# Kernel tuning notes

Measured on AMD Instinct MI355X. Metric: run time of the kernel, lower is better.

Reference implementation:

```python
import jax, jax.numpy as jnp
import numpy as np
from jax import lax

EMBED_DIM = 128
N_RELATIONS = 64
N_ENTITIES = 100000
N_EDGES = 600000


def setup_inputs() -> dict:
    key = jax.random.key(0)
    k1, k2, k3, k4, k5, k6 = jax.random.split(key, 6)
    entity_emb = jax.random.normal(k1, (N_ENTITIES, EMBED_DIM), dtype=jnp.float32)
    heads = jax.random.randint(k2, (N_EDGES,), 0, N_ENTITIES)
    rels = jax.random.randint(k3, (N_EDGES,), 0, N_RELATIONS)
    tails = jax.random.randint(k4, (N_EDGES,), 0, N_ENTITIES)
    # learned params: relation embedding table (std=0.01) and square Linear weight (xavier)
    rel_embed_weight = 0.01 * jax.random.normal(k5, (N_RELATIONS, EMBED_DIM), dtype=jnp.float32)
    xavier = float(np.sqrt(6.0 / (EMBED_DIM + EMBED_DIM)))
    W = jax.random.uniform(k6, (EMBED_DIM, EMBED_DIM), dtype=jnp.float32, minval=-xavier, maxval=xavier)
    return {"entity_emb": entity_emb, "rel_embed_weight": rel_embed_weight, "W": W,
            "heads": heads, "rels": rels, "tails": tails}


def reference(entity_emb, rel_embed_weight, W, heads, rels, tails):
    n_entities = entity_emb.shape[0]
    # gather edge endpoint / relation embeddings: [E, D]
    e_h = entity_emb[heads]
    e_t = entity_emb[tails]
    e_r = rel_embed_weight[rels]
    # tanh-gated dot-product score per edge: [E]
    score = jnp.sum(e_t * jnp.tanh(e_h + e_r), axis=-1)
    # global max-shift (detached in torch) then per-head segment softmax
    score_exp = jnp.exp(score - lax.stop_gradient(jnp.max(score)))
    score_sum = jax.ops.segment_sum(score_exp, heads, num_segments=n_entities)
    attn = score_exp / (score_sum[heads] + 1e-10)
    # scatter-add attention-weighted messages back to head nodes: [N, D]
    agg = jax.ops.segment_sum(attn[:, None] * e_t, heads, num_segments=n_entities)
    # final Linear (no bias) + LeakyReLU(0.2); dropout is identity in eval mode
    out = (entity_emb + agg) @ W.T
    return jax.nn.leaky_relu(out, negative_slope=0.2)
```

## Files before the change

kernel.cpp:

```cpp
#include <hip/hip_runtime.h>
#include <math.h>

#define EMBED 128
#define BMAX 8192
#define LDSPAD 136
#define DBINS 64

#define TWO_LOG2E 2.8853900817779268f
#define DEFER_THR 32.0f

typedef __attribute__((ext_vector_type(8))) short short8;
typedef __attribute__((ext_vector_type(4))) float floatx4;

__device__ __forceinline__ float ex2(float x) { return __builtin_amdgcn_exp2f(x); }

__device__ __forceinline__ float fast_tanh2(float x) {
    float e = ex2(TWO_LOG2E * x);
    return 1.0f - 2.0f * __builtin_amdgcn_rcpf(1.0f + e);
}

__device__ __forceinline__ unsigned short f2b(float f) {
    union { float f; unsigned int u; } v; v.f = f;
    unsigned int r = v.u + 0x7FFFu + ((v.u >> 16) & 1u);
    return (unsigned short)(r >> 16);
}

__device__ __forceinline__ float b2f(short u) {
    union { float f; unsigned int i; } v;
    v.i = ((unsigned int)(unsigned short)u) << 16;
    return v.f;
}

template <int CTRL>
__device__ __forceinline__ float dpp_add_f(float x) {
    int y = __builtin_amdgcn_update_dpp(0, __float_as_int(x), CTRL, 0xF, 0xF, false);
    return x + __int_as_float(y);
}
__device__ __forceinline__ float dpp_sum16(float s) {
    s = dpp_add_f<0x121>(s);
    s = dpp_add_f<0x122>(s);
    s = dpp_add_f<0x124>(s);
    s = dpp_add_f<0x128>(s);
    return s;
}

__global__ __launch_bounds__(256) void k_cast_hist(
    const float* __restrict__ ent, const float* __restrict__ rel, const float* __restrict__ W,
    short* __restrict__ entb, short* __restrict__ relb, short* __restrict__ wb,
    const int* __restrict__ heads, int* __restrict__ cnt, int* __restrict__ ghist,
    int ngE, int ngR, int ngW, int E)
{
    if (blockIdx.x == 0 && threadIdx.x < DBINS) ghist[threadIdx.x] = 0;
    int stride = gridDim.x * 256;
    int total = ngE + ngR + ngW;
    for (int g = blockIdx.x * 256 + threadIdx.x; g < total; g += stride) {
        const float4* src; short* dst;
        if (g < ngE)            { src = (const float4*)ent + (size_t)g * 2;              dst = entb + (size_t)g * 8; }
        else if (g < ngE + ngR) { int g2 = g - ngE;       src = (const float4*)rel + (size_t)g2 * 2; dst = relb + (size_t)g2 * 8; }
        else                    { int g2 = g - ngE - ngR; src = (const float4*)W   + (size_t)g2 * 2; dst = wb   + (size_t)g2 * 8; }
        float4 a = src[0], b = src[1];
        short8 o;
        o[0] = (short)f2b(a.x); o[1] = (short)f2b(a.y); o[2] = (short)f2b(a.z); o[3] = (short)f2b(a.w);
        o[4] = (short)f2b(b.x); o[5] = (short)f2b(b.y); o[6] = (short)f2b(b.z); o[7] = (short)f2b(b.w);
        *(short8*)dst = o;
    }
    for (int e = blockIdx.x * 256 + threadIdx.x; e < E; e += stride)
        atomicAdd(cnt + heads[e], 1);
}

__global__ __launch_bounds__(1024) void k_scan1(
    const int* __restrict__ cnt, int* __restrict__ offs,
    int* __restrict__ bsum, int* __restrict__ ghist, int N)
{
    __shared__ int wsum[16];
    __shared__ int dh[DBINS];
    const int tid = threadIdx.x;
    if (tid < DBINS) dh[tid] = 0;
    int i = blockIdx.x * 1024 + tid;
    int v = (i < N) ? cnt[i] : 0;
    __syncthreads();
    if (i < N) atomicAdd(&dh[v < DBINS ? v : DBINS - 1], 1);
    int x = v;
    #pragma unroll
    for (int d = 1; d < 64; d <<= 1) {
        int y = __shfl_up(x, d, 64);
        if ((tid & 63) >= d) x += y;
    }
    if ((tid & 63) == 63) wsum[tid >> 6] = x;
    __syncthreads();
    if (tid < 16) {
        int w = wsum[tid];
        #pragma unroll
        for (int d = 1; d < 16; d <<= 1) {
            int y = __shfl_up(w, d, 16);
            if (tid >= d) w += y;
        }
        wsum[tid] = w;
    }
    __syncthreads();
    int add = (tid >= 64) ? wsum[(tid >> 6) - 1] : 0;
    int incl = x + add;
    if (i < N) offs[i] = incl - v;
    if (tid == 1023) bsum[blockIdx.x] = incl;
    if (tid < DBINS && dh[tid] > 0) atomicAdd(ghist + tid, dh[tid]);
}

__global__ __launch_bounds__(256) void k_scan23(
    int* __restrict__ offs, const int* __restrict__ bsum,
    int* __restrict__ cursor, const int* __restrict__ cnt,
    const int* __restrict__ ghist, int* __restrict__ bincur,
    int* __restrict__ order, int N, int nb)
{
    __shared__ int sb[256];
    __shared__ int ws4[4];
    __shared__ int dbs[DBINS];
    __shared__ int lcnt[DBINS];
    __shared__ int lbase[DBINS];
    const int tid = threadIdx.x;

    int v = (tid < nb) ? bsum[tid] : 0;
    int x = v;
    #pragma unroll
    for (int d = 1; d < 64; d <<= 1) {
        int y = __shfl_up(x, d, 64);
        if ((tid & 63) >= d) x += y;
    }
    if ((tid & 63) == 63) ws4[tid >> 6] = x;
    __syncthreads();
    if (tid < 4) {
        int w = ws4[tid];
        #pragma unroll
        for (int d = 1; d < 4; d <<= 1) {
            int y = __shfl_up(w, d, 4);
            if (tid >= d) w += y;
        }
        ws4[tid] = w;
    }
    __syncthreads();
    int add = (tid >= 64) ? ws4[(tid >> 6) - 1] : 0;
    sb[tid] = x + add - v;

    if (tid < 64) {
        int g = ghist[tid];
        int s = g;
        #pragma unroll
        for (int d = 1; d < 64; d <<= 1) {
            int y = __shfl_up(s, d, 64);
            if (tid >= d) s += y;
        }
        dbs[tid] = s - g;
    }
    if (tid < DBINS) lcnt[tid] = 0;
    __syncthreads();

    int i = blockIdx.x * 256 + tid;
    int deg = 0, lrank = 0;
    if (i < N) {
        int o = offs[i] + sb[i >> 10];
        offs[i] = o;
        cursor[i] = o;
        int c = cnt[i];
        deg = c < DBINS ? c : DBINS - 1;
        lrank = atomicAdd(&lcnt[deg], 1);
    }
    __syncthreads();
    if (tid < DBINS) {
        int n = lcnt[tid];
        lbase[tid] = (n > 0) ? (dbs[tid] + atomicAdd(bincur + tid, n)) : 0;
    }
    __syncthreads();
    if (i < N) order[lbase[deg] + lrank] = i;
}

__global__ __launch_bounds__(256) void k_csr(
    const int* __restrict__ heads, const int* __restrict__ rels,
    const int* __restrict__ tails, int* __restrict__ cursor,
    int2* __restrict__ tr, int E)
{
    int e = blockIdx.x * 256 + threadIdx.x;
    if (e >= E) return;
    int pos = atomicAdd(cursor + heads[e], 1);
    tr[pos] = make_int2(tails[e], rels[e]);
}

__global__ __launch_bounds__(256) void k_fused(
    const short* __restrict__ entb, const short* __restrict__ relb,
    const int* __restrict__ offs, const int* __restrict__ cnt,
    const int2* __restrict__ tr, const int* __restrict__ order,
    short* __restrict__ accb, float* __restrict__ mh, float* __restrict__ lh,
    float* __restrict__ blockmax, int N, int R)
{
    const int tid = threadIdx.x;
    const int lane = tid & 15;
    int head0 = blockIdx.x * 16 + (tid >> 4);
    int head  = (head0 < N) ? order[(N - 1) - head0] : N;
    float mt = -INFINITY;
    if (head < N) {
        int start = offs[head];
        int c     = cnt[head];
        short8 hh = *((const short8*)(entb + (size_t)head * EMBED) + lane);
        float hf[8];
        #pragma unroll
        for (int i = 0; i < 8; ++i) hf[i] = b2f(hh[i]);
        float m = -INFINITY;
        float l = 0.f;
        float acc[8] = {0,0,0,0,0,0,0,0};
        for (int base = 0; base < c; base += 16) {
            int rem = c - base;
            int mm  = rem < 16 ? rem : 16;
            int2 trv = make_int2(0, 0);
            if (lane < mm) trv = tr[start + base + lane];
            int t0 = __shfl(trv.x, 0, 16);
            int r0 = __shfl(trv.y, 0, 16);
            short8 vtc = *((const short8*)(entb + (size_t)t0 * EMBED) + lane);
            short8 vrc = *((const short8*)(relb + (size_t)r0 * EMBED) + lane);
            for (int j = 0; j < mm; ++j) {
                int jn = (j + 1 < mm) ? j + 1 : j;
                int tn = __shfl(trv.x, jn, 16);
                int rn = __shfl(trv.y, jn, 16);
                short8 vtn = *((const short8*)(entb + (size_t)tn * EMBED) + lane);
                short8 vrn = *((const short8*)(relb + (size_t)rn * EMBED) + lane);
                float s = 0.f;
                float vtf[8];
                #pragma unroll
                for (int i = 0; i < 8; ++i) {
                    vtf[i] = b2f(vtc[i]);
                    s = fmaf(vtf[i], fast_tanh2(hf[i] + b2f(vrc[i])), s);
                }
                s = dpp_sum16(s);
                mt = fmaxf(mt, s);
                float dlt = s - m;
                if (dlt > DEFER_THR) {
                    float alpha = __expf(-dlt);
                    l *= alpha;
                    #pragma unroll
                    for (int q = 0; q < 8; ++q) acc[q] *= alpha;
                    m = s;
                    dlt = 0.f;
                }
                float p = __expf(dlt);
                l += p;
                #pragma unroll
                for (int q = 0; q < 8; ++q)
                    acc[q] = fmaf(p, vtf[q], acc[q]);
                vtc = vtn;
                vrc = vrn;
            }
        }
        short8 o;
        #pragma unroll
        for (int q = 0; q < 8; ++q) o[q] = (short)f2b(acc[q]);
        *((short8*)(accb + (size_t)head * EMBED) + lane) = o;
        if (lane == 0) { mh[head] = m; lh[head] = l; }
    }
    __shared__ float wmax[4];
    float wm = mt;
    #pragma unroll
    for (int off = 1; off < 64; off <<= 1) wm = fmaxf(wm, __shfl_xor(wm, off, 64));
    if ((tid & 63) == 0) wmax[tid >> 6] = wm;
    __syncthreads();
    if (tid == 0)
        blockmax[blockIdx.x] = fmaxf(fmaxf(wmax[0], wmax[1]), fmaxf(wmax[2], wmax[3]));
}

__global__ __launch_bounds__(256) void k_maxred(
    const float* __restrict__ blockmax, float* __restrict__ Mout, int n)
{
    __shared__ float smax[256];
    float m = -INFINITY;
    for (int i = threadIdx.x; i < n; i += 256) m = fmaxf(m, blockmax[i]);
    smax[threadIdx.x] = m;
    __syncthreads();
    for (int off = 128; off > 0; off >>= 1) {
        if ((int)threadIdx.x < off)
            smax[threadIdx.x] = fmaxf(smax[threadIdx.x], smax[threadIdx.x + off]);
        __syncthreads();
    }
    if (threadIdx.x == 0) Mout[0] = smax[0];
}

__global__ __launch_bounds__(256) void k_gemm_f(
    const short* __restrict__ entb, const short* __restrict__ accb,
    const float* __restrict__ mh, const float* __restrict__ lh,
    const float* __restrict__ Mptr, const short* __restrict__ wb,
    float* __restrict__ out, int N)
{
    __shared__ short xs[128 * LDSPAD];
    __shared__ short ws[128 * LDSPAD];
    __shared__ float invs[128];
    const int tid = threadIdx.x;
    const int n0  = blockIdx.x * 128;
    const float M = Mptr[0];

    if (tid < 128) {
        int g = n0 + tid;
        invs[tid] = (g < N) ? 1.0f / (lh[g] + 1e-10f * __expf(M - mh[g])) : 0.f;
    }
    #pragma unroll
    for (int it = 0; it < 8; ++it) {
        int ch = it * 256 + tid;
        int row = ch >> 4, col8 = ch & 15;
        *(short8*)(ws + row * LDSPAD + col8 * 8) = ((const short8*)wb)[ch];
    }
    __syncthreads();
    #pragma unroll
    for (int it = 0; it < 8; ++it) {
        int ch = it * 256 + tid;
        int row = ch >> 4, col8 = ch & 15;
        int g = n0 + row;
        short8 v = {0,0,0,0,0,0,0,0};
        if (g < N) {
            float inv = invs[row];
            short8 e8 = *((const short8*)(entb + (size_t)g * EMBED) + col8);
            short8 a8 = *((const short8*)(accb + (size_t)g * EMBED) + col8);
            #pragma unroll
            for (int q = 0; q < 8; ++q)
                v[q] = (short)f2b(b2f(e8[q]) + b2f(a8[q]) * inv);
        }
        *(short8*)(xs + row * LDSPAD + col8 * 8) = v;
    }
    __syncthreads();

    const int wv   = tid >> 6;
    const int lane = tid & 63;
    const int n16  = lane & 15;
    const int quad = lane >> 4;

    floatx4 acc[2][8];
    #pragma unroll
    for (int rt = 0; rt < 2; ++rt)
        #pragma unroll
        for (int jt = 0; jt < 8; ++jt)
            acc[rt][jt] = (floatx4){0.f, 0.f, 0.f, 0.f};

    #pragma unroll
    for (int kc = 0; kc < 4; ++kc) {
        int koff = kc * 32 + quad * 8;
        short8 a0 = *(const short8*)(xs + (wv * 32      + n16) * LDSPAD + koff);
        short8 a1 = *(const short8*)(xs + (wv * 32 + 16 + n16) * LDSPAD + koff);
        #pragma unroll
        for (int jt = 0; jt < 8; ++jt) {
            short8 b = *(const short8*)(ws + (jt * 16 + n16) * LDSPAD + koff);
            acc[0][jt] = __builtin_amdgcn_mfma_f32_16x16x32_bf16(a0, b, acc[0][jt], 0, 0, 0);
            acc[1][jt] = __builtin_amdgcn_mfma_f32_16x16x32_bf16(a1, b, acc[1][jt], 0, 0, 0);
        }
    }

    #pragma unroll
    for (int rt = 0; rt < 2; ++rt) {
        int rowbase = n0 + wv * 32 + rt * 16 + quad * 4;
        #pragma unroll
        for (int r = 0; r < 4; ++r) {
            int grow = rowbase + r;
            if (grow < N) {
                float* o = out + (size_t)grow * EMBED + n16;
                #pragma unroll
                for (int jt = 0; jt < 8; ++jt) {
                    float v = acc[rt][jt][r];
                    o[jt * 16] = (v > 0.f) ? v : 0.2f * v;
                }
            }
        }
    }
}

extern "C" void kernel_launch(void* const* d_in, const int* in_sizes, int n_in,
                              void* d_out, int out_size, void* d_ws, size_t ws_size,
                              hipStream_t stream)
{
    const float* ent   = (const float*)d_in[0];
    const float* rel   = (const float*)d_in[1];
    const float* W     = (const float*)d_in[2];
    const int*   heads = (const int*)d_in[3];
    const int*   rels  = (const int*)d_in[4];
    const int*   tails = (const int*)d_in[5];
    const int E = in_sizes[3];
    const int N = in_sizes[0] / EMBED;
    const int R = in_sizes[1] / EMBED;
    float* out = (float*)d_out;

    short* accb     = (short*)d_ws;
    float* mh       = (float*)(accb + (size_t)N * EMBED);
    float* lh       = mh + N;
    int2*  tr       = (int2*)(lh + N);
    int*   cnt      = (int*)(tr + E);
    int*   bincur   = cnt + N;
    int*   offs     = bincur + DBINS;
    int*   cursor   = offs + N;
    float* blockmax = (float*)(cursor + N);
    float* Mval     = blockmax + BMAX;
    int*   bsum     = (int*)(Mval + 4);
    int*   ghist    = bsum + 1024;
    int*   order    = ghist + DBINS;
    short* wb       = (short*)(order + N);
    short* entb     = wb + 16384;
    short* relb     = entb + (size_t)N * EMBED;

    const int nb  = (N + 1023) >> 10;
    const int ngh = (N + 15) / 16;

    hipMemsetAsync(cnt, 0, (size_t)(N + DBINS) * sizeof(int), stream);

    int ngE = N * EMBED / 8, ngR = R * EMBED / 8, ngW = EMBED * EMBED / 8;
    k_cast_hist<<<2048, 256, 0, stream>>>(ent, rel, W, entb, relb, wb, heads, cnt, ghist, ngE, ngR, ngW, E);
    k_scan1<<<nb, 1024, 0, stream>>>(cnt, offs, bsum, ghist, N);
    k_scan23<<<(N + 255) / 256, 256, 0, stream>>>(offs, bsum, cursor, cnt, ghist, bincur, order, N, nb);
    k_csr<<<(E + 255) / 256, 256, 0, stream>>>(heads, rels, tails, cursor, tr, E);
    k_fused<<<ngh, 256, 0, stream>>>(entb, relb, offs, cnt, tr, order, accb, mh, lh, blockmax, N, R);
    k_maxred<<<1, 256, 0, stream>>>(blockmax, Mval, ngh);
    k_gemm_f<<<(N + 127) / 128, 256, 0, stream>>>(entb, accb, mh, lh, Mval, wb, out, N);
}
```

Before: 238.5 us.

## Fold global max into atomicMax, prefetch edge indices, read W from global

Removes the separate max-reduction kernel. Each fused block now publishes its max through an order-preserving unsigned atomicMax on a word zeroed by the existing memset. The per-edge loop drops the 16-edge batching with shuffles and instead prefetches the tail/relation index pair two edges ahead directly from memory. The GEMM kernel stops staging W in LDS and reads B fragments straight from global/L2, which saves LDS but adds repeated global loads per block.

```diff
diff --git a/kernel.cpp b/kernel.cpp
--- a/kernel.cpp
+++ b/kernel.cpp
@@ -2,7 +2,6 @@
 #include <math.h>
 
 #define EMBED 128
-#define BMAX 8192
 #define LDSPAD 136
 #define DBINS 64
 
@@ -188,7 +187,7 @@
     const int* __restrict__ offs, const int* __restrict__ cnt,
     const int2* __restrict__ tr, const int* __restrict__ order,
     short* __restrict__ accb, float* __restrict__ mh, float* __restrict__ lh,
-    float* __restrict__ blockmax, int N, int R)
+    unsigned int* __restrict__ Mbits, int N)
 {
     const int tid = threadIdx.x;
     const int lane = tid & 15;
@@ -205,21 +204,16 @@
         float m = -INFINITY;
         float l = 0.f;
         float acc[8] = {0,0,0,0,0,0,0,0};
-        for (int base = 0; base < c; base += 16) {
-            int rem = c - base;
-            int mm  = rem < 16 ? rem : 16;
-            int2 trv = make_int2(0, 0);
-            if (lane < mm) trv = tr[start + base + lane];
-            int t0 = __shfl(trv.x, 0, 16);
-            int r0 = __shfl(trv.y, 0, 16);
-            short8 vtc = *((const short8*)(entb + (size_t)t0 * EMBED) + lane);
-            short8 vrc = *((const short8*)(relb + (size_t)r0 * EMBED) + lane);
-            for (int j = 0; j < mm; ++j) {
-                int jn = (j + 1 < mm) ? j + 1 : j;
-                int tn = __shfl(trv.x, jn, 16);
-                int rn = __shfl(trv.y, jn, 16);
-                short8 vtn = *((const short8*)(entb + (size_t)tn * EMBED) + lane);
-                short8 vrn = *((const short8*)(relb + (size_t)rn * EMBED) + lane);
+        if (c > 0) {
+            int2 tc = tr[start];
+            short8 vtc = *((const short8*)(entb + (size_t)tc.x * EMBED) + lane);
+            short8 vrc = *((const short8*)(relb + (size_t)tc.y * EMBED) + lane);
+            int2 tn = (c > 1) ? tr[start + 1] : tc;
+            for (int j = 0; j < c; ++j) {
+                short8 vtn = *((const short8*)(entb + (size_t)tn.x * EMBED) + lane);
+                short8 vrn = *((const short8*)(relb + (size_t)tn.y * EMBED) + lane);
+                int j2 = (j + 2 < c) ? j + 2 : c - 1;
+                int2 t2 = tr[start + j2];
                 float s = 0.f;
                 float vtf[8];
                 #pragma unroll
@@ -245,6 +239,7 @@
                     acc[q] = fmaf(p, vtf[q], acc[q]);
                 vtc = vtn;
                 vrc = vrn;
+                tn  = t2;
             }
         }
         short8 o;
@@ -259,48 +254,32 @@
     for (int off = 1; off < 64; off <<= 1) wm = fmaxf(wm, __shfl_xor(wm, off, 64));
     if ((tid & 63) == 0) wmax[tid >> 6] = wm;
     __syncthreads();
-    if (tid == 0)
-        blockmax[blockIdx.x] = fmaxf(fmaxf(wmax[0], wmax[1]), fmaxf(wmax[2], wmax[3]));
-}
-
-__global__ __launch_bounds__(256) void k_maxred(
-    const float* __restrict__ blockmax, float* __restrict__ Mout, int n)
-{
-    __shared__ float smax[256];
-    float m = -INFINITY;
-    for (int i = threadIdx.x; i < n; i += 256) m = fmaxf(m, blockmax[i]);
-    smax[threadIdx.x] = m;
-    __syncthreads();
-    for (int off = 128; off > 0; off >>= 1) {
-        if ((int)threadIdx.x < off)
-            smax[threadIdx.x] = fmaxf(smax[threadIdx.x], smax[threadIdx.x + off]);
-        __syncthreads();
-    }
-    if (threadIdx.x == 0) Mout[0] = smax[0];
+    if (tid == 0) {
+        float bm = fmaxf(fmaxf(wmax[0], wmax[1]), fmaxf(wmax[2], wmax[3]));
+        unsigned int u = __float_as_uint(bm);
+        unsigned int key = (u & 0x80000000u) ? ~u : (u | 0x80000000u);
+        if (key > *((volatile unsigned int*)Mbits))
+            atomicMax(Mbits, key);
+    }
 }
 
 __global__ __launch_bounds__(256) void k_gemm_f(
     const short* __restrict__ entb, const short* __restrict__ accb,
     const float* __restrict__ mh, const float* __restrict__ lh,
-    const float* __restrict__ Mptr, const short* __restrict__ wb,
+    const unsigned int* __restrict__ Mbits, const short* __restrict__ wb,
     float* __restrict__ out, int N)
 {
     __shared__ short xs[128 * LDSPAD];
-    __shared__ short ws[128 * LDSPAD];
     __shared__ float invs[128];
     const int tid = threadIdx.x;
     const int n0  = blockIdx.x * 128;
-    const float M = Mptr[0];
+    unsigned int k = Mbits[0];
+    const float M = (k & 0x80000000u) ? __uint_as_float(k & 0x7FFFFFFFu)
+                                      : __uint_as_float(~k);
 
     if (tid < 128) {
         int g = n0 + tid;
         invs[tid] = (g < N) ? 1.0f / (lh[g] + 1e-10f * __expf(M - mh[g])) : 0.f;
-    }
-    #pragma unroll
-    for (int it = 0; it < 8; ++it) {
-        int ch = it * 256 + tid;
-        int row = ch >> 4, col8 = ch & 15;
-        *(short8*)(ws + row * LDSPAD + col8 * 8) = ((const short8*)wb)[ch];
     }
     __syncthreads();
     #pragma unroll
@@ -340,7 +319,7 @@
         short8 a1 = *(const short8*)(xs + (wv * 32 + 16 + n16) * LDSPAD + koff);
         #pragma unroll
         for (int jt = 0; jt < 8; ++jt) {
-            short8 b = *(const short8*)(ws + (jt * 16 + n16) * LDSPAD + koff);
+            short8 b = *(const short8*)(wb + (jt * 16 + n16) * EMBED + koff);
             acc[0][jt] = __builtin_amdgcn_mfma_f32_16x16x32_bf16(a0, b, acc[0][jt], 0, 0, 0);
             acc[1][jt] = __builtin_amdgcn_mfma_f32_16x16x32_bf16(a1, b, acc[1][jt], 0, 0, 0);
         }
@@ -379,34 +358,32 @@
     const int R = in_sizes[1] / EMBED;
     float* out = (float*)d_out;
 
-    short* accb     = (short*)d_ws;
-    float* mh       = (float*)(accb + (size_t)N * EMBED);
-    float* lh       = mh + N;
-    int2*  tr       = (int2*)(lh + N);
-    int*   cnt      = (int*)(tr + E);
-    int*   bincur   = cnt + N;
-    int*   offs     = bincur + DBINS;
-    int*   cursor   = offs + N;
-    float* blockmax = (float*)(cursor + N);
-    float* Mval     = blockmax + BMAX;
-    int*   bsum     = (int*)(Mval + 4);
-    int*   ghist    = bsum + 1024;
-    int*   order    = ghist + DBINS;
-    short* wb       = (short*)(order + N);
-    short* entb     = wb + 16384;
-    short* relb     = entb + (size_t)N * EMBED;
+    short* accb      = (short*)d_ws;
+    float* mh        = (float*)(accb + (size_t)N * EMBED);
+    float* lh        = mh + N;
+    int2*  tr        = (int2*)(lh + N);
+    int*   cnt       = (int*)(tr + E);
+    int*   bincur    = cnt + N;
+    unsigned int* Mbits = (unsigned int*)(bincur + DBINS);
+    int*   offs      = (int*)(Mbits + 4);
+    int*   cursor    = offs + N;
+    int*   bsum      = cursor + N;
+    int*   ghist     = bsum + 1024;
+    int*   order     = ghist + DBINS;
+    short* wb        = (short*)(order + N);
+    short* entb      = wb + 16384;
+    short* relb      = entb + (size_t)N * EMBED;
 
     const int nb  = (N + 1023) >> 10;
     const int ngh = (N + 15) / 16;
 
-    hipMemsetAsync(cnt, 0, (size_t)(N + DBINS) * sizeof(int), stream);
+    hipMemsetAsync(cnt, 0, (size_t)(N + DBINS + 4) * sizeof(int), stream);
 
     int ngE = N * EMBED / 8, ngR = R * EMBED / 8, ngW = EMBED * EMBED / 8;
     k_cast_hist<<<2048, 256, 0, stream>>>(ent, rel, W, entb, relb, wb, heads, cnt, ghist, ngE, ngR, ngW, E);
     k_scan1<<<nb, 1024, 0, stream>>>(cnt, offs, bsum, ghist, N);
     k_scan23<<<(N + 255) / 256, 256, 0, stream>>>(offs, bsum, cursor, cnt, ghist, bincur, order, N, nb);
     k_csr<<<(E + 255) / 256, 256, 0, stream>>>(heads, rels, tails, cursor, tr, E);
-    k_fused<<<ngh, 256, 0, stream>>>(entb, relb, offs, cnt, tr, order, accb, mh, lh, blockmax, N, R);
-    k_maxred<<<1, 256, 0, stream>>>(blockmax, Mval, ngh);
-    k_gemm_f<<<(N + 127) / 128, 256, 0, stream>>>(entb, accb, mh, lh, Mval, wb, out, N);
-}
+    k_fused<<<ngh, 256, 0, stream>>>(entb, relb, offs, cnt, tr, order, accb, mh, lh, Mbits, N);
+    k_gemm_f<<<(N + 127) / 128, 256, 0, stream>>>(entb, accb, mh, lh, Mbits, wb, out, N);
+}
```

New measurement: 259.7 us. +8.9%, slower.
